# Optimization experiments

Measured on AMD Instinct MI355X. Metric: run time of the kernel, lower is better.

## Reference

```python
import jax, jax.numpy as jnp
import numpy as np

SEQ = 8192
EMB = 1024
MID = 1024


def setup_inputs() -> dict:
    key = jax.random.key(0)
    ks = jax.random.split(key, 7)
    s = 1.0 / np.sqrt(EMB)
    return {
        "text_encoded": jax.random.normal(ks[0], (SEQ, EMB), dtype=jnp.float32),
        "Wq": jax.random.normal(ks[1], (MID, EMB), dtype=jnp.float32) * s,
        "bq": jax.random.normal(ks[2], (MID,), dtype=jnp.float32) * 0.02,
        "Wk": jax.random.normal(ks[3], (MID, EMB), dtype=jnp.float32) * s,
        "bk": jax.random.normal(ks[4], (MID,), dtype=jnp.float32) * 0.02,
        "Wv": jax.random.normal(ks[5], (MID, EMB), dtype=jnp.float32) * s,
        "bv": jax.random.normal(ks[6], (MID,), dtype=jnp.float32) * 0.02,
    }


def reference(text_encoded, Wq, bq, Wk, bk, Wv, bv):
    # torch nn.Linear: y = x @ W.T + b, W is [out, in]
    Q = text_encoded @ Wq.T + bq  # [S, M]
    K = text_encoded @ Wk.T + bk  # [S, M]
    V = text_encoded @ Wv.T + bv  # [S, M]
    # cosine-similarity scores: (Q K^T) scaled by outer(1/||Q||, 1/||K||)
    inv_qn = jax.lax.rsqrt(jnp.sum(Q * Q, axis=1))  # [S]
    inv_kn = jax.lax.rsqrt(jnp.sum(K * K, axis=1))  # [S]
    scores = (Q @ K.T) * (inv_qn[:, None] * inv_kn[None, :])  # [S, S]
    weights = jax.nn.softmax(scores, axis=1)
    return weights @ V  # [S, M]
```

## Files before the change

kernel.cpp:

```cpp
#include <hip/hip_runtime.h>


#define SEQ 8192
#define MID 1024
#define EMB 1024

typedef __attribute__((ext_vector_type(8))) short short8x;
typedef __attribute__((ext_vector_type(16))) float float16x;
typedef __attribute__((ext_vector_type(4))) int int4x;
typedef __attribute__((ext_vector_type(16))) int int16x;

__device__ __forceinline__ unsigned short f2bf(float x) {
  union { float f; unsigned u; } v; v.f = x;
  unsigned r = v.u + 0x7FFFu + ((v.u >> 16) & 1u);
  return (unsigned short)(r >> 16);
}
__device__ __forceinline__ float bf2f(unsigned short h) {
  union { unsigned u; float f; } v; v.u = ((unsigned)h) << 16;
  return v.f;
}
__device__ __forceinline__ float fexp2(float x) {
#if __has_builtin(__builtin_amdgcn_exp2f)
  return __builtin_amdgcn_exp2f(x);
#else
  return __expf(x * 0.6931471805599453f);
#endif
}

__device__ __forceinline__ void g2l16(const void* g, void* lds) {
  __builtin_amdgcn_global_load_lds(
      (const __attribute__((address_space(1))) unsigned int*)g,
      (__attribute__((address_space(3))) unsigned int*)lds, 16, 0, 0);
}

__device__ __forceinline__ void gemm128_nt(
    const unsigned short* __restrict__ A, const unsigned short* __restrict__ B,
    long lda, long ldb, int m0, int n0, int K,
    unsigned short* As, unsigned short* Bs, float16x acc[2][2]) {
  const int tid = threadIdx.x;
  const int w = tid >> 6;
  const int l = tid & 63;
  const int wm = (w & 1) << 6;
  const int wn = (w >> 1) << 6;
  const int srow = l >> 3;
  const int skg = (l & 7) ^ srow;
  const int l31 = l & 31;
  const int lh = l >> 5;
  const int swz = l31 & 7;

  for (int k0 = 0; k0 < K; k0 += 64) {
    __syncthreads();
#pragma unroll
    for (int r = 0; r < 4; ++r) {
      const int rr = (w * 4 + r) * 8 + srow;
      g2l16(A + (long)(m0 + rr) * lda + k0 + skg * 8, As + (w * 4 + r) * 512);
      g2l16(B + (long)(n0 + rr) * ldb + k0 + skg * 8, Bs + (w * 4 + r) * 512);
    }
    __syncthreads();
#pragma unroll
    for (int ks = 0; ks < 4; ++ks) {
      const int kg = ks * 2 + lh;
      short8x av[2], bv[2];
#pragma unroll
      for (int t = 0; t < 2; ++t) {
        av[t] = *(const short8x*)(As + (wm + t * 32 + l31) * 64 + ((kg ^ swz) << 3));
        bv[t] = *(const short8x*)(Bs + (wn + t * 32 + l31) * 64 + ((kg ^ swz) << 3));
      }
#pragma unroll
      for (int tm = 0; tm < 2; ++tm)
#pragma unroll
        for (int tn = 0; tn < 2; ++tn)
          acc[tm][tn] = __builtin_amdgcn_mfma_f32_32x32x16_bf16(av[tm], bv[tn], acc[tm][tn], 0, 0, 0);
    }
  }
}

__device__ __forceinline__ void gemm128_nt_i8(
    const unsigned char* __restrict__ A, const unsigned char* __restrict__ B,
    long lda, long ldb, int m0, int n0, int Kbytes,
    unsigned char* As, unsigned char* Bs, int16x acc[2][2]) {
  const int tid = threadIdx.x;
  const int w = tid >> 6;
  const int l = tid & 63;
  const int wm = (w & 1) << 6;
  const int wn = (w >> 1) << 6;
  const int srow = l >> 3;
  const int skg = (l & 7) ^ srow;
  const int l31 = l & 31;
  const int lh = l >> 5;
  const int swz = l31 & 7;

  for (int k0 = 0; k0 < Kbytes; k0 += 128) {
    __syncthreads();
#pragma unroll
    for (int r = 0; r < 4; ++r) {
      const int rr = (w * 4 + r) * 8 + srow;
      g2l16(A + (long)(m0 + rr) * lda + k0 + skg * 16, As + (w * 4 + r) * 1024);
      g2l16(B + (long)(n0 + rr) * ldb + k0 + skg * 16, Bs + (w * 4 + r) * 1024);
    }
    __syncthreads();
#pragma unroll
    for (int ks = 0; ks < 4; ++ks) {
      const int kg = ks * 2 + lh;
      int4x av[2], bv[2];
#pragma unroll
      for (int t = 0; t < 2; ++t) {
        av[t] = *(const int4x*)(As + (wm + t * 32 + l31) * 128 + ((kg ^ swz) << 4));
        bv[t] = *(const int4x*)(Bs + (wn + t * 32 + l31) * 128 + ((kg ^ swz) << 4));
      }
#pragma unroll
      for (int tm = 0; tm < 2; ++tm)
#pragma unroll
        for (int tn = 0; tn < 2; ++tn)
          acc[tm][tn] = __builtin_amdgcn_mfma_i32_32x32x32_i8(av[tm], bv[tn], acc[tm][tn], 0, 0, 0);
    }
  }
}

__device__ __forceinline__ void gemm256x128_nt_i8(
    const unsigned char* __restrict__ A, const unsigned char* __restrict__ B,
    long lda, long ldb, int m0, int n0, int Kbytes,
    unsigned char* As, unsigned char* Bs, int16x acc[4][2]) {
  const int tid = threadIdx.x;
  const int w = tid >> 6;
  const int l = tid & 63;
  const int wm = (w & 1) << 7;
  const int wn = (w >> 1) << 6;
  const int srow = l >> 3;
  const int skg = (l & 7) ^ srow;
  const int l31 = l & 31;
  const int lh = l >> 5;
  const int swz = l31 & 7;

  for (int k0 = 0; k0 < Kbytes; k0 += 128) {
    __syncthreads();
#pragma unroll
    for (int r = 0; r < 8; ++r) {
      const int rr = (w * 8 + r) * 8 + srow;
      g2l16(A + (long)(m0 + rr) * lda + k0 + skg * 16, As + (w * 8 + r) * 1024);
    }
#pragma unroll
    for (int r = 0; r < 4; ++r) {
      const int rr = (w * 4 + r) * 8 + srow;
      g2l16(B + (long)(n0 + rr) * ldb + k0 + skg * 16, Bs + (w * 4 + r) * 1024);
    }
    __syncthreads();
#pragma unroll
    for (int ks = 0; ks < 4; ++ks) {
      const int kg = ks * 2 + lh;
      int4x av[4], bv[2];
#pragma unroll
      for (int t = 0; t < 4; ++t)
        av[t] = *(const int4x*)(As + (wm + t * 32 + l31) * 128 + ((kg ^ swz) << 4));
#pragma unroll
      for (int t = 0; t < 2; ++t)
        bv[t] = *(const int4x*)(Bs + (wn + t * 32 + l31) * 128 + ((kg ^ swz) << 4));
#pragma unroll
      for (int tm = 0; tm < 4; ++tm)
#pragma unroll
        for (int tn = 0; tn < 2; ++tn)
          acc[tm][tn] = __builtin_amdgcn_mfma_i32_32x32x32_i8(av[tm], bv[tn], acc[tm][tn], 0, 0, 0);
    }
  }
}

__global__ void cvt_all(const float* __restrict__ X,
                        const float* __restrict__ wq, const float* __restrict__ wk,
                        const float* __restrict__ wv,
                        unsigned short* __restrict__ Xb, unsigned short* __restrict__ Wb,
                        float* __restrict__ sums) {
  const long i = ((long)blockIdx.x * 256 + threadIdx.x) * 4;
  if (i < 24576) *(float4*)(sums + i) = (float4){0.f, 0.f, 0.f, 0.f};
  const float* src;
  unsigned short* dst;
  long off;
  if (i < (long)SEQ * EMB) {
    src = X; dst = Xb; off = i;
  } else {
    long j = i - (long)SEQ * EMB;
    int t = (int)(j >> 20);
    off = j & (MID * EMB - 1);
    src = (t == 0) ? wq : (t == 1) ? wk : wv;
    dst = Wb + (long)t * MID * EMB;
  }
  float4 v = *(const float4*)(src + off);
  ushort4 o;
  o.x = f2bf(v.x); o.y = f2bf(v.y); o.z = f2bf(v.z); o.w = f2bf(v.w);
  *(ushort4*)(dst + off) = o;
}

__global__ __launch_bounds__(256) void qkv_kernel(
    const unsigned short* __restrict__ Xb, const unsigned short* __restrict__ Wb,
    const float* __restrict__ bq, const float* __restrict__ bk, const float* __restrict__ bv,
    unsigned char* __restrict__ Q8, unsigned char* __restrict__ K8,
    unsigned char* __restrict__ VT8, float* __restrict__ sumsq) {
  __shared__ unsigned short smem[16384];
  unsigned short* As = smem;
  unsigned short* Bs = smem + 8192;
  const int z = blockIdx.z;
  const int mid0 = blockIdx.x * 128;
  const int seq0 = blockIdx.y * 128;
  float16x acc[2][2];
#pragma unroll
  for (int i = 0; i < 2; ++i)
#pragma unroll
    for (int j = 0; j < 2; ++j)
#pragma unroll
      for (int e = 0; e < 16; ++e) acc[i][j][e] = 0.f;

  if (z < 2) {
    gemm128_nt(Wb + (long)z * MID * EMB, Xb, EMB, EMB, mid0, seq0, EMB, As, Bs, acc);
  } else {
    gemm128_nt(Xb, Wb + 2l * MID * EMB, EMB, EMB, seq0, mid0, EMB, As, Bs, acc);
  }

  const int tid = threadIdx.x;
  const int l = tid & 63, w = tid >> 6;
  const int wm = (w & 1) << 6, wn = (w >> 1) << 6;
  const int l31 = l & 31, lh = l >> 5;

  __syncthreads();

  if (z < 2) {
    unsigned char* O8 = z ? K8 : Q8;
    const float* bias = z ? bk : bq;
    float* ss = sumsq + (long)z * SEQ;
    const float qs = 127.0f / 8.0f;
    float sq[2] = {0.f, 0.f};
    unsigned char* Plds = (unsigned char*)smem;
#pragma unroll
    for (int tm = 0; tm < 2; ++tm) {
#pragma unroll
      for (int g = 0; g < 4; ++g) {
        const int nb = wm + tm * 32 + g * 8 + lh * 4;
        float4 b4 = *(const float4*)(bias + mid0 + nb);
#pragma unroll
        for (int tn = 0; tn < 2; ++tn) {
          float t0 = fminf(127.f, fmaxf(-127.f, rintf((acc[tm][tn][g * 4 + 0] + b4.x) * qs)));
          float t1 = fminf(127.f, fmaxf(-127.f, rintf((acc[tm][tn][g * 4 + 1] + b4.y) * qs)));
          float t2 = fminf(127.f, fmaxf(-127.f, rintf((acc[tm][tn][g * 4 + 2] + b4.z) * qs)));
          float t3 = fminf(127.f, fmaxf(-127.f, rintf((acc[tm][tn][g * 4 + 3] + b4.w) * qs)));
          sq[tn] += t0 * t0 + t1 * t1 + t2 * t2 + t3 * t3;
          int q0 = (int)t0, q1 = (int)t1, q2 = (int)t2, q3 = (int)t3;
          unsigned pk = (q0 & 255) | ((q1 & 255) << 8) | ((q2 & 255) << 16) | ((q3 & 255) << 24);
          const int ml = wn + tn * 32 + l31;
          const int addr = ml * 128 + ((((nb >> 4) ^ (ml & 7)) << 4) | (nb & 15));
          *(unsigned*)(Plds + addr) = pk;
        }
      }
    }
#pragma unroll
    for (int tn = 0; tn < 2; ++tn) {
      float s = sq[tn] + __shfl_xor(sq[tn], 32);
      if (lh == 0) atomicAdd(ss + seq0 + wn + tn * 32 + l31, s);
    }
    __syncthreads();
#pragma unroll
    for (int round = 0; round < 4; ++round) {
      const int row = round * 32 + (tid >> 3);
      const int c = tid & 7;
      const int addr = row * 128 + ((c ^ (row & 7)) << 4);
      uint4 v = *(const uint4*)(Plds + addr);
      *(uint4*)(O8 + (long)(seq0 + row) * MID + mid0 + c * 16) = v;
    }
  } else {
    float bvv[2];
#pragma unroll
    for (int tn = 0; tn < 2; ++tn) bvv[tn] = bv[mid0 + wn + tn * 32 + l31];
#pragma unroll
    for (int tm = 0; tm < 2; ++tm)
#pragma unroll
      for (int tn = 0; tn < 2; ++tn)
#pragma unroll
        for (int r = 0; r < 16; ++r) acc[tm][tn][r] += bvv[tn];

#pragma unroll
    for (int tm = 0; tm < 2; ++tm)
#pragma unroll
      for (int tn = 0; tn < 2; ++tn) {
        const int nn = wn + tn * 32 + l31;
#pragma unroll
        for (int g = 0; g < 4; ++g) {
          const int mm = wm + tm * 32 + 8 * g + 4 * lh;
          const int chunk = (mm >> 3) ^ (nn & 7);
          ushort4 pk;
          pk.x = f2bf(acc[tm][tn][g * 4 + 0]);
          pk.y = f2bf(acc[tm][tn][g * 4 + 1]);
          pk.z = f2bf(acc[tm][tn][g * 4 + 2]);
          pk.w = f2bf(acc[tm][tn][g * 4 + 3]);
          *(ushort4*)(smem + nn * 128 + (chunk << 3) + (mm & 7)) = pk;
        }
      }
    __syncthreads();
    const float vs = 127.0f / 6.0f;
#pragma unroll
    for (int round = 0; round < 8; ++round) {
      const int nn = round * 16 + (tid >> 4);
      const int c = tid & 15;
      short8x vv = *(const short8x*)(smem + nn * 128 + ((c ^ (nn & 7)) << 3));
      int qq[8];
#pragma unroll
      for (int j = 0; j < 8; ++j) {
        float t = rintf(bf2f((unsigned short)vv[j]) * vs);
        t = fminf(127.f, fmaxf(-127.f, t));
        qq[j] = (int)t;
      }
      unsigned lo = (qq[0] & 255) | ((qq[1] & 255) << 8) | ((qq[2] & 255) << 16) | ((qq[3] & 255) << 24);
      unsigned hi = (qq[4] & 255) | ((qq[5] & 255) << 8) | ((qq[6] & 255) << 16) | ((qq[7] & 255) << 24);
      int2 pk; pk.x = (int)lo; pk.y = (int)hi;
      *(int2*)(VT8 + (long)(mid0 + nn) * SEQ + seq0 + c * 8) = pk;
    }
  }
}

__global__ __launch_bounds__(256, 2) void score_kernel(
    const unsigned char* __restrict__ Q8, const unsigned char* __restrict__ K8,
    const float* __restrict__ sumsq,
    unsigned char* __restrict__ P8, float* __restrict__ denomq) {
  __shared__ unsigned char smem8[49152];
  unsigned char* As = smem8;
  unsigned char* Bs = smem8 + 32768;
  const int kb0 = blockIdx.x * 256;
  const int qb0 = blockIdx.y * 128;
  int16x acc[4][2];
#pragma unroll
  for (int i = 0; i < 4; ++i)
#pragma unroll
    for (int j = 0; j < 2; ++j)
#pragma unroll
      for (int e = 0; e < 16; ++e) acc[i][j][e] = 0;

  gemm256x128_nt_i8(K8, Q8, MID, MID, kb0, qb0, MID, As, Bs, acc);

  const int tid = threadIdx.x;
  const int l = tid & 63, w = tid >> 6;
  const int wm = (w & 1) << 7, wn = (w >> 1) << 6;
  const int l31 = l & 31, lh = l >> 5;

  const float LOG2E  = 1.4426950408889634f;
  const float LOG2PS = 5.5459896458832860f;
  const float MAGIC  = 12582912.0f;
  float qi[2];
#pragma unroll
  for (int tn = 0; tn < 2; ++tn)
    qi[tn] = rsqrtf(sumsq[qb0 + wn + tn * 32 + l31]) * LOG2E;

  __syncthreads();

  unsigned char* Plds = As;
#pragma unroll
  for (int tm = 0; tm < 4; ++tm) {
#pragma unroll
    for (int g = 0; g < 4; ++g) {
      const int nb = wm + tm * 32 + g * 8 + lh * 4;
      float4 ss4 = *(const float4*)(sumsq + SEQ + kb0 + nb);
      float ik0 = rsqrtf(ss4.x), ik1 = rsqrtf(ss4.y);
      float ik2 = rsqrtf(ss4.z), ik3 = rsqrtf(ss4.w);
#pragma unroll
      for (int tn = 0; tn < 2; ++tn) {
        unsigned u0 = __float_as_uint(fexp2(fmaf((float)acc[tm][tn][g * 4 + 0] * ik0, qi[tn], LOG2PS)) + MAGIC);
        unsigned u1 = __float_as_uint(fexp2(fmaf((float)acc[tm][tn][g * 4 + 1] * ik1, qi[tn], LOG2PS)) + MAGIC);
        unsigned u2 = __float_as_uint(fexp2(fmaf((float)acc[tm][tn][g * 4 + 2] * ik2, qi[tn], LOG2PS)) + MAGIC);
        unsigned u3 = __float_as_uint(fexp2(fmaf((float)acc[tm][tn][g * 4 + 3] * ik3, qi[tn], LOG2PS)) + MAGIC);
        unsigned pk = (u0 & 255) | ((u1 & 255) << 8) | ((u2 & 255) << 16) | (u3 << 24);
        const int ml = wn + tn * 32 + l31;
        const int addr = ml * 256 + ((((nb >> 4) ^ (ml & 15)) << 4) | (nb & 15));
        *(unsigned*)(Plds + addr) = pk;
      }
    }
  }
  __syncthreads();

  const unsigned M8 = 0x00FF00FFu;
#pragma unroll
  for (int round = 0; round < 8; ++round) {
    const int row = round * 16 + (tid >> 4);
    const int c = tid & 15;
    const int addr = row * 256 + ((c ^ (row & 15)) << 4);
    uint4 v = *(const uint4*)(Plds + addr);
    unsigned e = (v.x & M8) + (v.y & M8) + (v.z & M8) + (v.w & M8);
    unsigned o = ((v.x >> 8) & M8) + ((v.y >> 8) & M8) + ((v.z >> 8) & M8) + ((v.w >> 8) & M8);
    unsigned t = e + o;
    unsigned s = (t & 0xFFFFu) + (t >> 16);
    *(uint4*)(P8 + (long)(qb0 + row) * SEQ + kb0 + c * 16) = v;
    s += __shfl_xor(s, 1); s += __shfl_xor(s, 2);
    s += __shfl_xor(s, 4); s += __shfl_xor(s, 8);
    if (c == 0) atomicAdd(denomq + qb0 + row, (float)s);
  }
}

__global__ __launch_bounds__(256, 4) void out_kernel(
    const unsigned char* __restrict__ P8, const unsigned char* __restrict__ VT8,
    const float* __restrict__ denomq, float* __restrict__ out) {
  __shared__ unsigned char smem8[32768];
  unsigned char* As = smem8;
  unsigned char* Bs = smem8 + 16384;
  const int m0 = blockIdx.x * 128;
  const int n0 = blockIdx.y * 128;
  int16x acc[2][2];
#pragma unroll
  for (int i = 0; i < 2; ++i)
#pragma unroll
    for (int j = 0; j < 2; ++j)
#pragma unroll
      for (int e = 0; e < 16; ++e) acc[i][j][e] = 0;

  gemm128_nt_i8(P8, VT8, SEQ, SEQ, m0, n0, SEQ, As, Bs, acc);

  const int l = threadIdx.x & 63, w = threadIdx.x >> 6;
  const int wm = (w & 1) << 6, wn = (w >> 1) << 6;
  const int l31 = l & 31, lh = l >> 5;
  const float sv = 127.0f / 6.0f;
#pragma unroll
  for (int tm = 0; tm < 2; ++tm)
#pragma unroll
    for (int r = 0; r < 16; ++r) {
      const int row = m0 + wm + tm * 32 + (r & 3) + 8 * (r >> 2) + 4 * lh;
      const float inv = 1.0f / (sv * denomq[row]);
#pragma unroll
      for (int tn = 0; tn < 2; ++tn) {
        const int col = n0 + wn + tn * 32 + l31;
        out[(long)row * MID + col] = (float)acc[tm][tn][r] * inv;
      }
    }
}

extern "C" void kernel_launch(void* const* d_in, const int* in_sizes, int n_in,
                              void* d_out, int out_size, void* d_ws, size_t ws_size,
                              hipStream_t stream) {
  const float* X  = (const float*)d_in[0];
  const float* Wq = (const float*)d_in[1];
  const float* bq = (const float*)d_in[2];
  const float* Wk = (const float*)d_in[3];
  const float* bk = (const float*)d_in[4];
  const float* Wv = (const float*)d_in[5];
  const float* bv = (const float*)d_in[6];

  char* wsb = (char*)d_ws;
  const size_t MB = 1ull << 20;
  unsigned char* Q8  = (unsigned char*)(wsb);
  unsigned char* K8  = (unsigned char*)(wsb + 8 * MB);
  unsigned char* VT8 = (unsigned char*)(wsb + 16 * MB);
  float* sums        = (float*)(wsb + 24 * MB);
  float* denomq      = sums + 2 * SEQ;
  unsigned char* P8  = (unsigned char*)(wsb + 25 * MB);
  unsigned short* Xb = (unsigned short*)(wsb + 25 * MB);
  unsigned short* Wb = (unsigned short*)(wsb + 41 * MB);

  const int cvt_elems = SEQ * EMB + 3 * MID * EMB;
  cvt_all<<<cvt_elems / 1024, 256, 0, stream>>>(X, Wq, Wk, Wv, Xb, Wb, sums);

  qkv_kernel<<<dim3(MID / 128, SEQ / 128, 3), 256, 0, stream>>>(Xb, Wb, bq, bk, bv, Q8, K8, VT8, sums);
  score_kernel<<<dim3(SEQ / 256, SEQ / 128), 256, 0, stream>>>(Q8, K8, sums, P8, denomq);
  out_kernel<<<dim3(SEQ / 128, MID / 128), 256, 0, stream>>>(P8, VT8, denomq, (float*)d_out);
}
```

Baseline: 341.3 us.

## Double-buffer int8 GEMM LDS staging and shrink score tiles to 128x128

Replaces the single-buffered int8 GEMM loops with one double-buffered version that prefetches the next K tile into the alternate LDS buffer while MFMAs run on the current one, leaving one barrier per iteration instead of two. The score kernel drops from 256x128 to 128x128 tiles, doubling its grid, and its P-tile LDS layout and row-sum reduction are adjusted to match. Both kernels now use 64KB of shared memory, and out_kernel's launch bound falls from 4 to 2 blocks per CU. This trades occupancy and score-GEMM tile reuse for overlap of global-to-LDS loads with compute.

```diff
diff --git a/kernel.cpp b/kernel.cpp
--- a/kernel.cpp
+++ b/kernel.cpp
@@ -75,10 +75,10 @@
   }
 }
 
-__device__ __forceinline__ void gemm128_nt_i8(
+__device__ __forceinline__ void gemm128_nt_i8_db(
     const unsigned char* __restrict__ A, const unsigned char* __restrict__ B,
     long lda, long ldb, int m0, int n0, int Kbytes,
-    unsigned char* As, unsigned char* Bs, int16x acc[2][2]) {
+    unsigned char* smem8, int16x acc[2][2]) {
   const int tid = threadIdx.x;
   const int w = tid >> 6;
   const int l = tid & 63;
@@ -90,15 +90,26 @@
   const int lh = l >> 5;
   const int swz = l31 & 7;
 
-  for (int k0 = 0; k0 < Kbytes; k0 += 128) {
-    __syncthreads();
-#pragma unroll
-    for (int r = 0; r < 4; ++r) {
-      const int rr = (w * 4 + r) * 8 + srow;
-      g2l16(A + (long)(m0 + rr) * lda + k0 + skg * 16, As + (w * 4 + r) * 1024);
-      g2l16(B + (long)(n0 + rr) * ldb + k0 + skg * 16, Bs + (w * 4 + r) * 1024);
-    }
-    __syncthreads();
+#define STAGE_DB(kt_) do {                                                              \
+    unsigned char* As_ = smem8 + (((kt_) & 1) << 14);                                   \
+    unsigned char* Bs_ = smem8 + 32768 + (((kt_) & 1) << 14);                           \
+    const int k0_ = (kt_) << 7;                                                         \
+    _Pragma("unroll")                                                                   \
+    for (int r = 0; r < 4; ++r) {                                                       \
+      const int rr = (w * 4 + r) * 8 + srow;                                            \
+      g2l16(A + (long)(m0 + rr) * lda + k0_ + skg * 16, As_ + (w * 4 + r) * 1024);      \
+      g2l16(B + (long)(n0 + rr) * ldb + k0_ + skg * 16, Bs_ + (w * 4 + r) * 1024);      \
+    }                                                                                   \
+  } while (0)
+
+  const int nk = Kbytes >> 7;
+  STAGE_DB(0);
+  __syncthreads();
+#pragma unroll 1
+  for (int kt = 0; kt < nk; ++kt) {
+    unsigned char* As = smem8 + ((kt & 1) << 14);
+    unsigned char* Bs = smem8 + 32768 + ((kt & 1) << 14);
+    if (kt + 1 < nk) STAGE_DB(kt + 1);
 #pragma unroll
     for (int ks = 0; ks < 4; ++ks) {
       const int kg = ks * 2 + lh;
@@ -114,54 +125,9 @@
         for (int tn = 0; tn < 2; ++tn)
           acc[tm][tn] = __builtin_amdgcn_mfma_i32_32x32x32_i8(av[tm], bv[tn], acc[tm][tn], 0, 0, 0);
     }
-  }
-}
-
-__device__ __forceinline__ void gemm256x128_nt_i8(
-    const unsigned char* __restrict__ A, const unsigned char* __restrict__ B,
-    long lda, long ldb, int m0, int n0, int Kbytes,
-    unsigned char* As, unsigned char* Bs, int16x acc[4][2]) {
-  const int tid = threadIdx.x;
-  const int w = tid >> 6;
-  const int l = tid & 63;
-  const int wm = (w & 1) << 7;
-  const int wn = (w >> 1) << 6;
-  const int srow = l >> 3;
-  const int skg = (l & 7) ^ srow;
-  const int l31 = l & 31;
-  const int lh = l >> 5;
-  const int swz = l31 & 7;
-
-  for (int k0 = 0; k0 < Kbytes; k0 += 128) {
     __syncthreads();
-#pragma unroll
-    for (int r = 0; r < 8; ++r) {
-      const int rr = (w * 8 + r) * 8 + srow;
-      g2l16(A + (long)(m0 + rr) * lda + k0 + skg * 16, As + (w * 8 + r) * 1024);
-    }
-#pragma unroll
-    for (int r = 0; r < 4; ++r) {
-      const int rr = (w * 4 + r) * 8 + srow;
-      g2l16(B + (long)(n0 + rr) * ldb + k0 + skg * 16, Bs + (w * 4 + r) * 1024);
-    }
-    __syncthreads();
-#pragma unroll
-    for (int ks = 0; ks < 4; ++ks) {
-      const int kg = ks * 2 + lh;
-      int4x av[4], bv[2];
-#pragma unroll
-      for (int t = 0; t < 4; ++t)
-        av[t] = *(const int4x*)(As + (wm + t * 32 + l31) * 128 + ((kg ^ swz) << 4));
-#pragma unroll
-      for (int t = 0; t < 2; ++t)
-        bv[t] = *(const int4x*)(Bs + (wn + t * 32 + l31) * 128 + ((kg ^ swz) << 4));
-#pragma unroll
-      for (int tm = 0; tm < 4; ++tm)
-#pragma unroll
-        for (int tn = 0; tn < 2; ++tn)
-          acc[tm][tn] = __builtin_amdgcn_mfma_i32_32x32x32_i8(av[tm], bv[tn], acc[tm][tn], 0, 0, 0);
-    }
-  }
+  }
+#undef STAGE_DB
 }
 
 __global__ void cvt_all(const float* __restrict__ X,
@@ -317,24 +283,22 @@
     const unsigned char* __restrict__ Q8, const unsigned char* __restrict__ K8,
     const float* __restrict__ sumsq,
     unsigned char* __restrict__ P8, float* __restrict__ denomq) {
-  __shared__ unsigned char smem8[49152];
-  unsigned char* As = smem8;
-  unsigned char* Bs = smem8 + 32768;
-  const int kb0 = blockIdx.x * 256;
+  __shared__ unsigned char smem8[65536];
+  const int kb0 = blockIdx.x * 128;
   const int qb0 = blockIdx.y * 128;
-  int16x acc[4][2];
-#pragma unroll
-  for (int i = 0; i < 4; ++i)
+  int16x acc[2][2];
+#pragma unroll
+  for (int i = 0; i < 2; ++i)
 #pragma unroll
     for (int j = 0; j < 2; ++j)
 #pragma unroll
       for (int e = 0; e < 16; ++e) acc[i][j][e] = 0;
 
-  gemm256x128_nt_i8(K8, Q8, MID, MID, kb0, qb0, MID, As, Bs, acc);
+  gemm128_nt_i8_db(K8, Q8, MID, MID, kb0, qb0, MID, smem8, acc);
 
   const int tid = threadIdx.x;
   const int l = tid & 63, w = tid >> 6;
-  const int wm = (w & 1) << 7, wn = (w >> 1) << 6;
+  const int wm = (w & 1) << 6, wn = (w >> 1) << 6;
   const int l31 = l & 31, lh = l >> 5;
 
   const float LOG2E  = 1.4426950408889634f;
@@ -345,11 +309,9 @@
   for (int tn = 0; tn < 2; ++tn)
     qi[tn] = rsqrtf(sumsq[qb0 + wn + tn * 32 + l31]) * LOG2E;
 
-  __syncthreads();
-
-  unsigned char* Plds = As;
-#pragma unroll
-  for (int tm = 0; tm < 4; ++tm) {
+  unsigned char* Plds = smem8;
+#pragma unroll
+  for (int tm = 0; tm < 2; ++tm) {
 #pragma unroll
     for (int g = 0; g < 4; ++g) {
       const int nb = wm + tm * 32 + g * 8 + lh * 4;
@@ -364,7 +326,7 @@
         unsigned u3 = __float_as_uint(fexp2(fmaf((float)acc[tm][tn][g * 4 + 3] * ik3, qi[tn], LOG2PS)) + MAGIC);
         unsigned pk = (u0 & 255) | ((u1 & 255) << 8) | ((u2 & 255) << 16) | (u3 << 24);
         const int ml = wn + tn * 32 + l31;
-        const int addr = ml * 256 + ((((nb >> 4) ^ (ml & 15)) << 4) | (nb & 15));
+        const int addr = ml * 128 + ((((nb >> 4) ^ (ml & 7)) << 4) | (nb & 15));
         *(unsigned*)(Plds + addr) = pk;
       }
     }
@@ -373,28 +335,25 @@
 
   const unsigned M8 = 0x00FF00FFu;
 #pragma unroll
-  for (int round = 0; round < 8; ++round) {
-    const int row = round * 16 + (tid >> 4);
-    const int c = tid & 15;
-    const int addr = row * 256 + ((c ^ (row & 15)) << 4);
+  for (int round = 0; round < 4; ++round) {
+    const int row = round * 32 + (tid >> 3);
+    const int c = tid & 7;
+    const int addr = row * 128 + ((c ^ (row & 7)) << 4);
     uint4 v = *(const uint4*)(Plds + addr);
     unsigned e = (v.x & M8) + (v.y & M8) + (v.z & M8) + (v.w & M8);
     unsigned o = ((v.x >> 8) & M8) + ((v.y >> 8) & M8) + ((v.z >> 8) & M8) + ((v.w >> 8) & M8);
     unsigned t = e + o;
     unsigned s = (t & 0xFFFFu) + (t >> 16);
     *(uint4*)(P8 + (long)(qb0 + row) * SEQ + kb0 + c * 16) = v;
-    s += __shfl_xor(s, 1); s += __shfl_xor(s, 2);
-    s += __shfl_xor(s, 4); s += __shfl_xor(s, 8);
+    s += __shfl_xor(s, 1); s += __shfl_xor(s, 2); s += __shfl_xor(s, 4);
     if (c == 0) atomicAdd(denomq + qb0 + row, (float)s);
   }
 }
 
-__global__ __launch_bounds__(256, 4) void out_kernel(
+__global__ __launch_bounds__(256, 2) void out_kernel(
     const unsigned char* __restrict__ P8, const unsigned char* __restrict__ VT8,
     const float* __restrict__ denomq, float* __restrict__ out) {
-  __shared__ unsigned char smem8[32768];
-  unsigned char* As = smem8;
-  unsigned char* Bs = smem8 + 16384;
+  __shared__ unsigned char smem8[65536];
   const int m0 = blockIdx.x * 128;
   const int n0 = blockIdx.y * 128;
   int16x acc[2][2];
@@ -405,7 +364,7 @@
 #pragma unroll
       for (int e = 0; e < 16; ++e) acc[i][j][e] = 0;
 
-  gemm128_nt_i8(P8, VT8, SEQ, SEQ, m0, n0, SEQ, As, Bs, acc);
+  gemm128_nt_i8_db(P8, VT8, SEQ, SEQ, m0, n0, SEQ, smem8, acc);
 
   const int l = threadIdx.x & 63, w = threadIdx.x >> 6;
   const int wm = (w & 1) << 6, wn = (w >> 1) << 6;
@@ -451,6 +410,6 @@
   cvt_all<<<cvt_elems / 1024, 256, 0, stream>>>(X, Wq, Wk, Wv, Xb, Wb, sums);
 
   qkv_kernel<<<dim3(MID / 128, SEQ / 128, 3), 256, 0, stream>>>(Xb, Wb, bq, bk, bv, Q8, K8, VT8, sums);
-  score_kernel<<<dim3(SEQ / 256, SEQ / 128), 256, 0, stream>>>(Q8, K8, sums, P8, denomq);
+  score_kernel<<<dim3(SEQ / 128, SEQ / 128), 256, 0, stream>>>(Q8, K8, sums, P8, denomq);
   out_kernel<<<dim3(SEQ / 128, MID / 128), 256, 0, stream>>>(P8, VT8, denomq, (float*)d_out);
 }
```

New measurement: 330.4 us. 1.03x faster.
